# Performance work log

Hardware: AMD Instinct MI355X
Metric: run time of the kernel (lower is better)

Reference implementation:

```python
import jax, jax.numpy as jnp
import numpy as np

N, G, K, D = 16, 4096, 8, 2  # agents, grid points (64x64 flattened), fiber dim, manifold dim


def setup_inputs() -> dict:
    key = jax.random.key(0)
    k0, k1, k2, k3 = jax.random.split(key, 4)
    I = jnp.eye(K, dtype=jnp.float32)
    # frames and links: identity + small perturbation (invertible, as init_twist_scale=0.05 implies)
    omega = I + 0.05 * jax.random.normal(k0, (N, G, K, K), dtype=jnp.float32)
    links = I + 0.05 * jax.random.normal(k1, (N, D, G, K, K), dtype=jnp.float32)
    mu_q = jax.random.normal(k2, (N, G, K), dtype=jnp.float32)
    A = 0.3 * jax.random.normal(k3, (N, G, K, K), dtype=jnp.float32)
    sigma_q = A @ A.swapaxes(-1, -2) + I  # SPD covariances
    return {"omega": omega, "links": links, "mu_q": mu_q, "sigma_q": sigma_q}


def reference(omega, links, mu_q, sigma_q):
    """pairwise_alignment_with_twists: E[i,j,g] = KL(q_i || Omega_ij[q_j]).

    full_transport: Omega_ij = omega_i @ V_i @ inv(omega_j),
    V_i = I + sum_d (link_{i,d} - I)   (links depend only on i, per source).
    """
    I = jnp.eye(K, dtype=omega.dtype)
    V = I + jnp.sum(links - I, axis=1)                       # (N,G,K,K)
    T = omega @ V                                            # omega_i V_i, (N,G,K,K)
    omega_inv = jnp.linalg.inv(omega)                        # (N,G,K,K)
    Om = jnp.einsum('igab,jgbc->ijgac', T, omega_inv)        # (N,N,G,K,K)

    mu_t = jnp.einsum('ijgab,jgb->ijga', Om, mu_q)           # transported means
    sig_t = jnp.einsum('ijgab,jgbc,ijgdc->ijgad', Om, sigma_q, Om)  # Om Sigma Om^T

    inv2 = jnp.linalg.inv(sig_t)                             # Sigma2^{-1}
    diff = mu_t - mu_q[:, None]                              # (N,N,G,K)
    tr = jnp.einsum('ijgab,igba->ijg', inv2, sigma_q)        # tr(Sigma2^{-1} Sigma1)
    quad = jnp.einsum('ijga,ijgab,ijgb->ijg', diff, inv2, diff)
    ld2 = jnp.linalg.slogdet(sig_t)[1]                       # (N,N,G)
    ld1 = jnp.linalg.slogdet(sigma_q)[1]                     # (N,G)
    E = 0.5 * (tr + quad - K + ld2 - ld1[:, None, :])
    # zero the diagonal (i == j skipped in the original loop)
    mask = 1.0 - jnp.eye(N, dtype=E.dtype)
    return E * mask[:, :, None]
```

## Files before the change

### kernel.cpp

```cpp
#include <hip/hip_runtime.h>
#include <math.h>

#define NN 16
#define GG 4096
#define STR 76
#define SSTR 68
#define NWG GG

template <int CTRL>
__device__ __forceinline__ float dppf(float x) {
    return __builtin_bit_cast(float, __builtin_amdgcn_mov_dpp(
        __builtin_bit_cast(int, x), CTRL, 0xF, 0xF, true));
}
__device__ __forceinline__ float qb(float x, int L) {
    switch (L) {
        case 0:  return dppf<0x00>(x);
        case 1:  return dppf<0x55>(x);
        case 2:  return dppf<0xAA>(x);
        default: return dppf<0xFF>(x);
    }
}
__device__ __forceinline__ float qsum(float x) {
    x += dppf<0xB1>(x);
    x += dppf<0x4E>(x);
    return x;
}
__device__ __forceinline__ void bcast_row(float out[8], const float r0[8],
                                          const float r1[8], int k) {
#pragma unroll
    for (int c = 0; c < 8; ++c) {
        float s = (k < 4) ? r0[c] : r1[c];
        out[c] = qb(s, k & 3);
    }
}
__device__ __forceinline__ float sel_lo(const float r[8], int q) {
    return (q == 0) ? r[0] : (q == 1) ? r[1] : (q == 2) ? r[2] : r[3];
}
__device__ __forceinline__ float sel_hi(const float r[8], int q) {
    return (q == 0) ? r[4] : (q == 1) ? r[5] : (q == 2) ? r[6] : r[7];
}
__device__ __forceinline__ void ld_row(float r[8], const float* p) {
    float4 x = *(const float4*)p, y = *(const float4*)(p + 4);
    r[0] = x.x; r[1] = x.y; r[2] = x.z; r[3] = x.w;
    r[4] = y.x; r[5] = y.y; r[6] = y.z; r[7] = y.w;
}
__device__ __forceinline__ void st_row(float* p, const float r[8]) {
    *(float4*)p       = make_float4(r[0], r[1], r[2], r[3]);
    *(float4*)(p + 4) = make_float4(r[4], r[5], r[6], r[7]);
}
__device__ __forceinline__ float dot8(const float a[8], const float b[8]) {
    float s = a[0] * b[0];
    s = fmaf(a[1], b[1], s); s = fmaf(a[2], b[2], s);
    s = fmaf(a[3], b[3], s); s = fmaf(a[4], b[4], s);
    s = fmaf(a[5], b[5], s); s = fmaf(a[6], b[6], s);
    s = fmaf(a[7], b[7], s);
    return s;
}

__device__ __forceinline__ float gj4(float r0[8], float r1[8], int q) {
    float pp = 1.0f;
#pragma unroll
    for (int k = 0; k < 8; ++k) {
        float Mk[8];
        bcast_row(Mk, r0, r1, k);
        float p = Mk[k];
        pp *= p;
        float ip = 1.0f / p;
        bool own0 = (k < 4) && (q == k);
        bool own1 = (k >= 4) && (q == k - 4);
        float m0 = -(own0 ? -1.0f : r0[k]) * ip;
        float m1 = -(own1 ? -1.0f : r1[k]) * ip;
#pragma unroll
        for (int c = 0; c < 8; ++c) {
            float b0 = own0 ? 0.0f : r0[c];
            float b1 = own1 ? 0.0f : r1[c];
            r0[c] = fmaf(m0, Mk[c], b0);
            r1[c] = fmaf(m1, Mk[c], b1);
        }
        r0[k] = m0;
        r1[k] = m1;
    }
    return pp;
}

__device__ __forceinline__ float ludet4(float r0[8], float r1[8], int q) {
    float pp = 1.0f;
#pragma unroll
    for (int k = 0; k < 8; ++k) {
        float Mk[8];
#pragma unroll
        for (int c = k; c < 8; ++c) {
            float s = (k < 4) ? r0[c] : r1[c];
            Mk[c] = qb(s, k & 3);
        }
        float p = Mk[k];
        pp *= p;
        float ip = 1.0f / p;
        float f0 = (q > k) ? r0[k] * ip : 0.f;
        float f1 = (q + 4 > k) ? r1[k] * ip : 0.f;
#pragma unroll
        for (int c = k + 1; c < 8; ++c) {
            r0[c] = fmaf(-f0, Mk[c], r0[c]);
            r1[c] = fmaf(-f1, Mk[c], r1[c]);
        }
    }
    return pp;
}

__global__ __launch_bounds__(64) void pairkl_kernel(
    const float* __restrict__ omega, const float* __restrict__ links,
    const float* __restrict__ mu, const float* __restrict__ sigma,
    float* __restrict__ out) {
    __shared__ __align__(16) float sh_x[NN][STR];
    __shared__ __align__(16) float sh_y[NN][STR];
    float* sh_s = &sh_y[0][0];

    const int bid  = blockIdx.x;
    const int g    = (bid & 7) * (NWG / 8) + (bid >> 3);
    const int lane = threadIdx.x;
    const int item = lane >> 2;
    const int q    = lane & 3;
    const int mb   = (item * GG + g) * 64;

    float v0[8], v1[8], o0[8], o1[8], mq[8];
    {
        const float* l0p = links + ((item * 2 + 0) * GG + g) * 64;
        const float* l1p = links + ((item * 2 + 1) * GG + g) * 64;
        float la[8], lb[8];
        ld_row(la, l0p + q * 8);
        ld_row(lb, l1p + q * 8);
#pragma unroll
        for (int c = 0; c < 8; ++c) v0[c] = la[c] + lb[c] - ((c == q) ? 1.f : 0.f);
        ld_row(la, l0p + (q + 4) * 8);
        ld_row(lb, l1p + (q + 4) * 8);
#pragma unroll
        for (int c = 0; c < 8; ++c) v1[c] = la[c] + lb[c] - ((c == q + 4) ? 1.f : 0.f);
    }
    ld_row(o0, omega + mb + q * 8);
    ld_row(o1, omega + mb + (q + 4) * 8);
    {
        float sa[8], sb[8];
        ld_row(sa, sigma + mb + q * 8);
        ld_row(sb, sigma + mb + (q + 4) * 8);
        st_row(&sh_s[item * SSTR + q * 8], sa);
        st_row(&sh_s[item * SSTR + (q + 4) * 8], sb);
    }
    ld_row(mq, mu + (item * GG + g) * 8);

    float R0[8], R1[8];
#pragma unroll
    for (int c = 0; c < 8; ++c) { R0[c] = 0.f; R1[c] = 0.f; }
#pragma unroll
    for (int b = 0; b < 8; ++b) {
        float Vb[8]; bcast_row(Vb, v0, v1, b);
#pragma unroll
        for (int c = 0; c < 8; ++c) {
            R0[c] = fmaf(o0[b], Vb[c], R0[c]);
            R1[c] = fmaf(o1[b], Vb[c], R1[c]);
        }
    }
    float ldV = logf(fabsf(ludet4(v0, v1, q)));
    float ldT = logf(fabsf(gj4(R0, R1, q)));
    float Z0[8], Z1[8];
#pragma unroll
    for (int c = 0; c < 8; ++c) { Z0[c] = 0.f; Z1[c] = 0.f; }
#pragma unroll
    for (int b = 0; b < 8; ++b) {
        float sr[8]; ld_row(sr, &sh_s[item * SSTR + b * 8]);
#pragma unroll
        for (int c = 0; c < 8; ++c) {
            Z0[c] = fmaf(R0[b], sr[c], Z0[c]);
            Z1[c] = fmaf(R1[b], sr[c], Z1[c]);
        }
    }
    float u_lo = dot8(R0, mq), u_hi = dot8(R1, mq);
    float uf[8];
#pragma unroll
    for (int c = 0; c < 4; ++c) { uf[c] = qb(u_lo, c); uf[c + 4] = qb(u_hi, c); }
#pragma unroll
    for (int c = 0; c < 8; ++c) {
        float Wc[8]; bcast_row(Wc, R0, R1, c);
        v0[c] = fmaf(u_lo, uf[c], dot8(Z0, Wc));
        v1[c] = fmaf(u_hi, uf[c], dot8(Z1, Wc));
    }
    st_row(&sh_x[item][q * 8], v0);
    st_row(&sh_x[item][(q + 4) * 8], v1);

    float s0[8], s1[8];
    ld_row(s0, &sh_s[item * SSTR + q * 8]);
    ld_row(s1, &sh_s[item * SSTR + (q + 4) * 8]);
    float ld1 = logf(fabsf(gj4(s0, s1, q)));
    float mql = sel_lo(mq, q), mqh = sel_hi(mq, q);
    float cc  = qsum(dot8(s0, mq) * mql + dot8(s1, mq) * mqh);
    float U0[8], U1[8];
#pragma unroll
    for (int c = 0; c < 8; ++c) { U0[c] = 0.f; U1[c] = 0.f; }
#pragma unroll
    for (int b = 0; b < 8; ++b) {
        float Ob[8]; bcast_row(Ob, o0, o1, b);
#pragma unroll
        for (int c = 0; c < 8; ++c) {
            U0[c] = fmaf(s0[b], Ob[c], U0[c]);
            U1[c] = fmaf(s1[b], Ob[c], U1[c]);
        }
    }
    float wf[8];
#pragma unroll
    for (int c = 0; c < 8; ++c) wf[c] = qsum(fmaf(mql, U0[c], mqh * U1[c]));
    float oc0[8], oc1[8];
#pragma unroll
    for (int a = 0; a < 8; ++a) {
        oc0[a] = omega[mb + a * 8 + q];
        oc1[a] = omega[mb + a * 8 + q + 4];
    }
#pragma unroll
    for (int c = 0; c < 8; ++c) { s0[c] = 0.f; s1[c] = 0.f; }
#pragma unroll
    for (int a = 0; a < 8; ++a) {
        float Ua[8]; bcast_row(Ua, U0, U1, a);
#pragma unroll
        for (int c = 0; c < 8; ++c) {
            s0[c] = fmaf(oc0[a], Ua[c], s0[c]);
            s1[c] = fmaf(oc1[a], Ua[c], s1[c]);
        }
    }
    st_row(&sh_y[item][q * 8], s0);
    st_row(&sh_y[item][(q + 4) * 8], s1);

    if (q == 0) {
        float ldo = ldT - ldV;
        float a_i = 2.f * ldT - ld1;
        float s_j = ld1 - 2.f * ldo + cc - 8.0f;
        *(float4*)&sh_x[item][64] = make_float4(uf[0], uf[1], uf[2], uf[3]);
        *(float4*)&sh_x[item][68] = make_float4(uf[4], uf[5], uf[6], uf[7]);
        *(float4*)&sh_x[item][72] = make_float4(a_i, 1.f, 0.f, 0.f);
        *(float4*)&sh_y[item][64] =
            make_float4(-2.f * wf[0], -2.f * wf[1], -2.f * wf[2], -2.f * wf[3]);
        *(float4*)&sh_y[item][68] =
            make_float4(-2.f * wf[4], -2.f * wf[5], -2.f * wf[6], -2.f * wf[7]);
        *(float4*)&sh_y[item][72] = make_float4(1.f, s_j, 0.f, 0.f);
    }
    asm volatile("" ::: "memory");

    {
        const int i0 = lane >> 3, j0 = lane & 7;
        const int i1 = i0 + 8, j1 = j0 + 8;
        const float4* x0 = (const float4*)&sh_x[i0][0];
        const float4* x1 = (const float4*)&sh_x[i1][0];
        const float4* y0 = (const float4*)&sh_y[j0][0];
        const float4* y1 = (const float4*)&sh_y[j1][0];
        float d00 = 0.f, d01 = 0.f, d10 = 0.f, d11 = 0.f;
#pragma unroll
        for (int k = 0; k < STR / 4; ++k) {
            float4 a0 = x0[k], a1 = x1[k], b0 = y0[k], b1 = y1[k];
            d00 = fmaf(a0.x, b0.x, d00); d00 = fmaf(a0.y, b0.y, d00);
            d00 = fmaf(a0.z, b0.z, d00); d00 = fmaf(a0.w, b0.w, d00);
            d01 = fmaf(a0.x, b1.x, d01); d01 = fmaf(a0.y, b1.y, d01);
            d01 = fmaf(a0.z, b1.z, d01); d01 = fmaf(a0.w, b1.w, d01);
            d10 = fmaf(a1.x, b0.x, d10); d10 = fmaf(a1.y, b0.y, d10);
            d10 = fmaf(a1.z, b0.z, d10); d10 = fmaf(a1.w, b0.w, d10);
            d11 = fmaf(a1.x, b1.x, d11); d11 = fmaf(a1.y, b1.y, d11);
            d11 = fmaf(a1.z, b1.z, d11); d11 = fmaf(a1.w, b1.w, d11);
        }
        const bool dg = (i0 == j0);
        out[(i0 * NN + j0) * GG + g] = dg ? 0.f : 0.5f * d00;
        out[(i0 * NN + j1) * GG + g] = 0.5f * d01;
        out[(i1 * NN + j0) * GG + g] = 0.5f * d10;
        out[(i1 * NN + j1) * GG + g] = dg ? 0.f : 0.5f * d11;
    }
}

extern "C" void kernel_launch(void* const* d_in, const int* in_sizes, int n_in,
                              void* d_out, int out_size, void* d_ws, size_t ws_size,
                              hipStream_t stream) {
    const float* omega = (const float*)d_in[0];
    const float* links = (const float*)d_in[1];
    const float* mu    = (const float*)d_in[2];
    const float* sigma = (const float*)d_in[3];
    float* out = (float*)d_out;
    hipLaunchKernelGGL(pairkl_kernel, dim3(NWG), dim3(64), 0, stream,
                       omega, links, mu, sigma, out);
}
```

Measured before the change: 27.65 us.

## Pack symmetric matrices into upper-triangle form and process two grid points per block

The final pairwise dot product now uses the symmetry of the 8x8 matrices. Only the diagonal and doubled upper-triangle entries are stored, which cuts the shared-memory vector length from 76 to 48 floats. Each block now runs two wavefronts on two grid points, halving the block count. The V matrix is built row-by-row from global loads instead of DPP broadcasts, and sigma and omega rows are reread from global/cache instead of being staged in shared memory. This trades extra global-load traffic and branchy scattered LDS stores for fewer FMAs in the reduction and fewer cross-lane ops.

```diff
diff --git a/kernel.cpp b/kernel.cpp
--- a/kernel.cpp
+++ b/kernel.cpp
@@ -3,9 +3,8 @@
 
 #define NN 16
 #define GG 4096
-#define STR 76
-#define SSTR 68
-#define NWG GG
+#define XSTR 52
+#define NWG (GG / 2)
 
 template <int CTRL>
 __device__ __forceinline__ float dppf(float x) {
@@ -33,20 +32,19 @@
         out[c] = qb(s, k & 3);
     }
 }
+__device__ __forceinline__ float sel4(float a, float b, float c, float d, int k) {
+    return (k == 0) ? a : (k == 1) ? b : (k == 2) ? c : d;
+}
 __device__ __forceinline__ float sel_lo(const float r[8], int q) {
-    return (q == 0) ? r[0] : (q == 1) ? r[1] : (q == 2) ? r[2] : r[3];
+    return sel4(r[0], r[1], r[2], r[3], q);
 }
 __device__ __forceinline__ float sel_hi(const float r[8], int q) {
-    return (q == 0) ? r[4] : (q == 1) ? r[5] : (q == 2) ? r[6] : r[7];
+    return sel4(r[4], r[5], r[6], r[7], q);
 }
 __device__ __forceinline__ void ld_row(float r[8], const float* p) {
     float4 x = *(const float4*)p, y = *(const float4*)(p + 4);
     r[0] = x.x; r[1] = x.y; r[2] = x.z; r[3] = x.w;
     r[4] = y.x; r[5] = y.y; r[6] = y.z; r[7] = y.w;
-}
-__device__ __forceinline__ void st_row(float* p, const float r[8]) {
-    *(float4*)p       = make_float4(r[0], r[1], r[2], r[3]);
-    *(float4*)(p + 4) = make_float4(r[4], r[5], r[6], r[7]);
 }
 __device__ __forceinline__ float dot8(const float a[8], const float b[8]) {
     float s = a[0] * b[0];
@@ -107,26 +105,51 @@
     return pp;
 }
 
-__global__ __launch_bounds__(64) void pairkl_kernel(
+__global__ __launch_bounds__(128) void pairkl_kernel(
     const float* __restrict__ omega, const float* __restrict__ links,
     const float* __restrict__ mu, const float* __restrict__ sigma,
     float* __restrict__ out) {
-    __shared__ __align__(16) float sh_x[NN][STR];
-    __shared__ __align__(16) float sh_y[NN][STR];
-    float* sh_s = &sh_y[0][0];
+    __shared__ __align__(16) float sh_x[2][NN][XSTR];
+    __shared__ __align__(16) float sh_y[2][NN][XSTR];
 
     const int bid  = blockIdx.x;
-    const int g    = (bid & 7) * (NWG / 8) + (bid >> 3);
-    const int lane = threadIdx.x;
+    const int work = (bid & 7) * (NWG / 8) + (bid >> 3);
+    const int t    = threadIdx.x;
+    const int w    = t >> 6;
+    const int g    = work * 2 + w;
+    const int lane = t & 63;
     const int item = lane >> 2;
     const int q    = lane & 3;
     const int mb   = (item * GG + g) * 64;
-
-    float v0[8], v1[8], o0[8], o1[8], mq[8];
-    {
-        const float* l0p = links + ((item * 2 + 0) * GG + g) * 64;
-        const float* l1p = links + ((item * 2 + 1) * GG + g) * 64;
-        float la[8], lb[8];
+    const float* l0p = links + ((item * 2 + 0) * GG + g) * 64;
+    const float* l1p = links + ((item * 2 + 1) * GG + g) * 64;
+
+    float mq[8];
+    ld_row(mq, mu + (item * GG + g) * 8);
+
+    float R0[8], R1[8];
+    {
+        float o0[8], o1[8];
+        ld_row(o0, omega + mb + q * 8);
+        ld_row(o1, omega + mb + (q + 4) * 8);
+#pragma unroll
+        for (int c = 0; c < 8; ++c) { R0[c] = 0.f; R1[c] = 0.f; }
+#pragma unroll
+        for (int b = 0; b < 8; ++b) {
+            float la[8], lb[8];
+            ld_row(la, l0p + b * 8);
+            ld_row(lb, l1p + b * 8);
+#pragma unroll
+            for (int c = 0; c < 8; ++c) {
+                float vb = la[c] + lb[c] - ((c == b) ? 1.f : 0.f);
+                R0[c] = fmaf(o0[b], vb, R0[c]);
+                R1[c] = fmaf(o1[b], vb, R1[c]);
+            }
+        }
+    }
+    float ldV;
+    {
+        float v0[8], v1[8], la[8], lb[8];
         ld_row(la, l0p + q * 8);
         ld_row(lb, l1p + q * 8);
 #pragma unroll
@@ -135,38 +158,16 @@
         ld_row(lb, l1p + (q + 4) * 8);
 #pragma unroll
         for (int c = 0; c < 8; ++c) v1[c] = la[c] + lb[c] - ((c == q + 4) ? 1.f : 0.f);
-    }
-    ld_row(o0, omega + mb + q * 8);
-    ld_row(o1, omega + mb + (q + 4) * 8);
-    {
-        float sa[8], sb[8];
-        ld_row(sa, sigma + mb + q * 8);
-        ld_row(sb, sigma + mb + (q + 4) * 8);
-        st_row(&sh_s[item * SSTR + q * 8], sa);
-        st_row(&sh_s[item * SSTR + (q + 4) * 8], sb);
-    }
-    ld_row(mq, mu + (item * GG + g) * 8);
-
-    float R0[8], R1[8];
-#pragma unroll
-    for (int c = 0; c < 8; ++c) { R0[c] = 0.f; R1[c] = 0.f; }
-#pragma unroll
-    for (int b = 0; b < 8; ++b) {
-        float Vb[8]; bcast_row(Vb, v0, v1, b);
-#pragma unroll
-        for (int c = 0; c < 8; ++c) {
-            R0[c] = fmaf(o0[b], Vb[c], R0[c]);
-            R1[c] = fmaf(o1[b], Vb[c], R1[c]);
-        }
-    }
-    float ldV = logf(fabsf(ludet4(v0, v1, q)));
+        ldV = logf(fabsf(ludet4(v0, v1, q)));
+    }
     float ldT = logf(fabsf(gj4(R0, R1, q)));
     float Z0[8], Z1[8];
 #pragma unroll
     for (int c = 0; c < 8; ++c) { Z0[c] = 0.f; Z1[c] = 0.f; }
 #pragma unroll
     for (int b = 0; b < 8; ++b) {
-        float sr[8]; ld_row(sr, &sh_s[item * SSTR + b * 8]);
+        float sr[8];
+        ld_row(sr, sigma + mb + b * 8);
 #pragma unroll
         for (int c = 0; c < 8; ++c) {
             Z0[c] = fmaf(R0[b], sr[c], Z0[c]);
@@ -177,18 +178,35 @@
     float uf[8];
 #pragma unroll
     for (int c = 0; c < 4; ++c) { uf[c] = qb(u_lo, c); uf[c + 4] = qb(u_hi, c); }
-#pragma unroll
-    for (int c = 0; c < 8; ++c) {
-        float Wc[8]; bcast_row(Wc, R0, R1, c);
-        v0[c] = fmaf(u_lo, uf[c], dot8(Z0, Wc));
-        v1[c] = fmaf(u_hi, uf[c], dot8(Z1, Wc));
-    }
-    st_row(&sh_x[item][q * 8], v0);
-    st_row(&sh_x[item][(q + 4) * 8], v1);
+    {
+        float X0[8], X1[8];
+#pragma unroll
+        for (int c = 0; c < 8; ++c) {
+            float Wc[8]; bcast_row(Wc, R0, R1, c);
+            X0[c] = fmaf(u_lo, uf[c], dot8(Z0, Wc));
+            X1[c] = fmaf(u_hi, uf[c], dot8(Z1, Wc));
+        }
+        float* xb = &sh_x[w][item][0];
+        xb[q]     = sel4(X0[0], X0[1], X0[2], X0[3], q);
+        xb[q + 4] = sel4(X1[4], X1[5], X1[6], X1[7], q);
+        const int basea = 7 + 6 * q - ((q * (q - 1)) >> 1);
+        const int a2 = q + 4;
+        const int baseb = 7 + 6 * a2 - ((a2 * (a2 - 1)) >> 1);
+#pragma unroll
+        for (int b = 1; b < 8; ++b)
+            if (b > q) xb[basea + b] = 2.f * X0[b];
+#pragma unroll
+        for (int b = 5; b < 8; ++b)
+            if (b > a2) xb[baseb + b] = 2.f * X1[b];
+        if (q == 0) {
+            *(float4*)&xb[36] = make_float4(uf[0], uf[1], uf[2], uf[3]);
+            *(float4*)&xb[40] = make_float4(uf[4], uf[5], uf[6], uf[7]);
+        }
+    }
 
     float s0[8], s1[8];
-    ld_row(s0, &sh_s[item * SSTR + q * 8]);
-    ld_row(s1, &sh_s[item * SSTR + (q + 4) * 8]);
+    ld_row(s0, sigma + mb + q * 8);
+    ld_row(s1, sigma + mb + (q + 4) * 8);
     float ld1 = logf(fabsf(gj4(s0, s1, q)));
     float mql = sel_lo(mq, q), mqh = sel_hi(mq, q);
     float cc  = qsum(dot8(s0, mq) * mql + dot8(s1, mq) * mqh);
@@ -197,61 +215,72 @@
     for (int c = 0; c < 8; ++c) { U0[c] = 0.f; U1[c] = 0.f; }
 #pragma unroll
     for (int b = 0; b < 8; ++b) {
-        float Ob[8]; bcast_row(Ob, o0, o1, b);
+        float orow[8];
+        ld_row(orow, omega + mb + b * 8);
 #pragma unroll
         for (int c = 0; c < 8; ++c) {
-            U0[c] = fmaf(s0[b], Ob[c], U0[c]);
-            U1[c] = fmaf(s1[b], Ob[c], U1[c]);
+            U0[c] = fmaf(s0[b], orow[c], U0[c]);
+            U1[c] = fmaf(s1[b], orow[c], U1[c]);
         }
     }
     float wf[8];
 #pragma unroll
     for (int c = 0; c < 8; ++c) wf[c] = qsum(fmaf(mql, U0[c], mqh * U1[c]));
-    float oc0[8], oc1[8];
-#pragma unroll
-    for (int a = 0; a < 8; ++a) {
-        oc0[a] = omega[mb + a * 8 + q];
-        oc1[a] = omega[mb + a * 8 + q + 4];
-    }
-#pragma unroll
-    for (int c = 0; c < 8; ++c) { s0[c] = 0.f; s1[c] = 0.f; }
-#pragma unroll
-    for (int a = 0; a < 8; ++a) {
-        float Ua[8]; bcast_row(Ua, U0, U1, a);
-#pragma unroll
-        for (int c = 0; c < 8; ++c) {
-            s0[c] = fmaf(oc0[a], Ua[c], s0[c]);
-            s1[c] = fmaf(oc1[a], Ua[c], s1[c]);
-        }
-    }
-    st_row(&sh_y[item][q * 8], s0);
-    st_row(&sh_y[item][(q + 4) * 8], s1);
-
-    if (q == 0) {
-        float ldo = ldT - ldV;
-        float a_i = 2.f * ldT - ld1;
-        float s_j = ld1 - 2.f * ldo + cc - 8.0f;
-        *(float4*)&sh_x[item][64] = make_float4(uf[0], uf[1], uf[2], uf[3]);
-        *(float4*)&sh_x[item][68] = make_float4(uf[4], uf[5], uf[6], uf[7]);
-        *(float4*)&sh_x[item][72] = make_float4(a_i, 1.f, 0.f, 0.f);
-        *(float4*)&sh_y[item][64] =
-            make_float4(-2.f * wf[0], -2.f * wf[1], -2.f * wf[2], -2.f * wf[3]);
-        *(float4*)&sh_y[item][68] =
-            make_float4(-2.f * wf[4], -2.f * wf[5], -2.f * wf[6], -2.f * wf[7]);
-        *(float4*)&sh_y[item][72] = make_float4(1.f, s_j, 0.f, 0.f);
+    {
+        float oc0[8], oc1[8];
+#pragma unroll
+        for (int a = 0; a < 8; ++a) {
+            oc0[a] = omega[mb + a * 8 + q];
+            oc1[a] = omega[mb + a * 8 + q + 4];
+        }
+        float P0[8], P1[8];
+#pragma unroll
+        for (int c = 0; c < 8; ++c) { P0[c] = 0.f; P1[c] = 0.f; }
+#pragma unroll
+        for (int a = 0; a < 8; ++a) {
+            float Ua[8]; bcast_row(Ua, U0, U1, a);
+#pragma unroll
+            for (int c = 0; c < 8; ++c) {
+                P0[c] = fmaf(oc0[a], Ua[c], P0[c]);
+                P1[c] = fmaf(oc1[a], Ua[c], P1[c]);
+            }
+        }
+        float* yb = &sh_y[w][item][0];
+        yb[q]     = sel4(P0[0], P0[1], P0[2], P0[3], q);
+        yb[q + 4] = sel4(P1[4], P1[5], P1[6], P1[7], q);
+        const int basea = 7 + 6 * q - ((q * (q - 1)) >> 1);
+        const int a2 = q + 4;
+        const int baseb = 7 + 6 * a2 - ((a2 * (a2 - 1)) >> 1);
+#pragma unroll
+        for (int b = 1; b < 8; ++b)
+            if (b > q) yb[basea + b] = P0[b];
+#pragma unroll
+        for (int b = 5; b < 8; ++b)
+            if (b > a2) yb[baseb + b] = P1[b];
+        if (q == 0) {
+            float ldo = ldT - ldV;
+            float a_i = 2.f * ldT - ld1;
+            float s_j = ld1 - 2.f * ldo + cc - 8.0f;
+            *(float4*)&yb[36] =
+                make_float4(-2.f * wf[0], -2.f * wf[1], -2.f * wf[2], -2.f * wf[3]);
+            *(float4*)&yb[40] =
+                make_float4(-2.f * wf[4], -2.f * wf[5], -2.f * wf[6], -2.f * wf[7]);
+            *(float4*)&yb[44] = make_float4(1.f, s_j, 0.f, 0.f);
+            *(float4*)&sh_x[w][item][44] = make_float4(a_i, 1.f, 0.f, 0.f);
+        }
     }
     asm volatile("" ::: "memory");
 
     {
         const int i0 = lane >> 3, j0 = lane & 7;
         const int i1 = i0 + 8, j1 = j0 + 8;
-        const float4* x0 = (const float4*)&sh_x[i0][0];
-        const float4* x1 = (const float4*)&sh_x[i1][0];
-        const float4* y0 = (const float4*)&sh_y[j0][0];
-        const float4* y1 = (const float4*)&sh_y[j1][0];
+        const float4* x0 = (const float4*)&sh_x[w][i0][0];
+        const float4* x1 = (const float4*)&sh_x[w][i1][0];
+        const float4* y0 = (const float4*)&sh_y[w][j0][0];
+        const float4* y1 = (const float4*)&sh_y[w][j1][0];
         float d00 = 0.f, d01 = 0.f, d10 = 0.f, d11 = 0.f;
 #pragma unroll
-        for (int k = 0; k < STR / 4; ++k) {
+        for (int k = 0; k < 12; ++k) {
             float4 a0 = x0[k], a1 = x1[k], b0 = y0[k], b1 = y1[k];
             d00 = fmaf(a0.x, b0.x, d00); d00 = fmaf(a0.y, b0.y, d00);
             d00 = fmaf(a0.z, b0.z, d00); d00 = fmaf(a0.w, b0.w, d00);
@@ -278,6 +307,6 @@
     const float* mu    = (const float*)d_in[2];
     const float* sigma = (const float*)d_in[3];
     float* out = (float*)d_out;
-    hipLaunchKernelGGL(pairkl_kernel, dim3(NWG), dim3(64), 0, stream,
+    hipLaunchKernelGGL(pairkl_kernel, dim3(NWG), dim3(128), 0, stream,
                        omega, links, mu, sigma, out);
 }
```

Measured after the change: 29.99 us. 1.08x slower.
